# Kernel optimization log

Measured on AMD Instinct MI355X. Metric: run time of the kernel, lower is better.

## Reference

```python
import jax, jax.numpy as jnp
import numpy as np

B, S, T, D, H, K, F = 8, 512, 512, 1024, 16, 64, 4096
EPS = 1e-6
NEG = -1e9


def _ln(x, g, b):
    mu = jnp.mean(x, axis=-1, keepdims=True)
    var = jnp.mean(jnp.square(x - mu), axis=-1, keepdims=True)
    return (x - mu) * jax.lax.rsqrt(var + EPS) * g + b


def _mha(q_in, kv_in, wq, bq, wk, bk, wv, bv, wo, bo, mask=None):
    # q_in: [B,S,D], kv_in: [B,T,D]
    q = jnp.einsum('bsd,dhk->bshk', q_in, wq) + bq
    k = jnp.einsum('btd,dhk->bthk', kv_in, wk) + bk
    v = jnp.einsum('btd,dhk->bthk', kv_in, wv) + bv
    scores = jnp.einsum('bshk,bthk->bhst', q, k) / jnp.sqrt(jnp.float32(K))
    if mask is not None:
        scores = jnp.where(mask, scores, NEG)
    attn = jax.nn.softmax(scores, axis=-1)  # [B,H,S,T]
    ctx = jnp.einsum('bhst,bthk->bshk', attn, v)
    out = jnp.einsum('bshk,hkd->bsd', ctx, wo) + bo
    return out, attn


def setup_inputs() -> dict:
    key = jax.random.key(0)
    ks = jax.random.split(key, 24)
    r = lambda i, shape: 0.02 * jax.random.normal(ks[i], shape, dtype=jnp.float32)
    inp = {
        'x': jax.random.normal(ks[0], (B, S, D), dtype=jnp.float32),
        'enc_output': jax.random.normal(ks[1], (B, T, D), dtype=jnp.float32),
        'look_ahead_mask': jnp.tril(jnp.ones((S, S), dtype=bool))[None, None],
        # mha1 (self-attention)
        'wq1': r(2, (D, H, K)), 'bq1': jnp.zeros((H, K), jnp.float32),
        'wk1': r(3, (D, H, K)), 'bk1': jnp.zeros((H, K), jnp.float32),
        'wv1': r(4, (D, H, K)), 'bv1': jnp.zeros((H, K), jnp.float32),
        'wo1': r(5, (H, K, D)), 'bo1': jnp.zeros((D,), jnp.float32),
        # mha2 (cross-attention)
        'wq2': r(6, (D, H, K)), 'bq2': jnp.zeros((H, K), jnp.float32),
        'wk2': r(7, (D, H, K)), 'bk2': jnp.zeros((H, K), jnp.float32),
        'wv2': r(8, (D, H, K)), 'bv2': jnp.zeros((H, K), jnp.float32),
        'wo2': r(9, (H, K, D)), 'bo2': jnp.zeros((D,), jnp.float32),
        # layernorms
        'g1': jnp.ones((D,), jnp.float32), 'be1': jnp.zeros((D,), jnp.float32),
        'g2': jnp.ones((D,), jnp.float32), 'be2': jnp.zeros((D,), jnp.float32),
        'g3': jnp.ones((D,), jnp.float32), 'be3': jnp.zeros((D,), jnp.float32),
        # ffn
        'w_fc1': r(10, (D, F)), 'b_fc1': jnp.zeros((F,), jnp.float32),
        'w_fc2': r(11, (F, D)), 'b_fc2': jnp.zeros((D,), jnp.float32),
    }
    return inp


def reference(x, enc_output, look_ahead_mask,
              wq1, bq1, wk1, bk1, wv1, bv1, wo1, bo1,
              wq2, bq2, wk2, bk2, wv2, bv2, wo2, bo2,
              g1, be1, g2, be2, g3, be3,
              w_fc1, b_fc1, w_fc2, b_fc2):
    attn1, attn_w1 = _mha(x, x, wq1, bq1, wk1, bk1, wv1, bv1, wo1, bo1,
                          mask=look_ahead_mask)
    out1 = _ln(attn1 + x, g1, be1)
    attn2, attn_w2 = _mha(out1, enc_output, wq2, bq2, wk2, bk2, wv2, bv2, wo2, bo2)
    out2 = _ln(attn2 + out1, g2, be2)
    h = jax.nn.relu(jnp.einsum('bsd,df->bsf', out2, w_fc1) + b_fc1)
    out_ffn = jnp.einsum('bsf,fd->bsd', h, w_fc2) + b_fc2
    dec_layer_out = _ln(out_ffn + out2, g3, be3)
    return dec_layer_out, attn_w1, attn_w2
```

## Files before the change

kernel.cpp:

```cpp
#include <hip/hip_runtime.h>

typedef __attribute__((ext_vector_type(4))) float f32x4;
typedef __attribute__((ext_vector_type(8))) __bf16 bf16x8;

__device__ __forceinline__ unsigned short f2b(float f){
  union { float f; unsigned int u; } v; v.f = f;
  unsigned int r = v.u + 0x7FFFu + ((v.u >> 16) & 1u);
  return (unsigned short)(r >> 16);
}
__device__ __forceinline__ float b2f(unsigned short u){
  union { unsigned int u; float f; } v; v.u = ((unsigned int)u) << 16;
  return v.f;
}
__device__ __forceinline__ bool in_is_bf16(const void* g1){
  return ((const unsigned short*)g1)[0] == 0x3F80u;
}

#define GLD16(gp, lp) __builtin_amdgcn_global_load_lds( \
    (const __attribute__((address_space(1))) unsigned int*)(gp), \
    (__attribute__((address_space(3))) unsigned int*)(lp), 16, 0, 0)

__device__ __forceinline__ int xcd_swz(int L, int nwg){
  return (L & 7) * (nwg >> 3) + (L >> 3);
}

__global__ __launch_bounds__(256) void k_fill(float* p, long long n, float v){
  long long i = (long long)blockIdx.x*256 + threadIdx.x;
  long long stride = (long long)gridDim.x*256;
  for(; i < n; i += stride) p[i] = v;
}

struct SmallConv { const void* src[16]; int n[16]; int off[16]; };
struct TW4 { const void* s[4]; };

template<bool SMALL>
__global__ __launch_bounds__(256) void k_prepA(SmallConv sc, float* bias,
    const void* act_in, unsigned short* act_out,
    TW4 tw, unsigned short* wdst, const void* g1f)
{
  __shared__ float tile[32][33];
  bool isb = in_is_bf16(g1f);
  int bi = blockIdx.x, tid = threadIdx.x;
  int base = SMALL ? 16 : 0;
  if(SMALL && bi < 16){
    const void* s = sc.src[bi];
    float* d = bias + sc.off[bi];
    int n = sc.n[bi];
    for(int j=tid;j<n;j+=256)
      d[j] = isb ? b2f(((const unsigned short*)s)[j]) : ((const float*)s)[j];
  } else if(bi < base + 2048){
    for(int i=(bi-base)*256+tid; i<4194304; i+=2048*256){
      float v = isb ? b2f(((const unsigned short*)act_in)[i]) : ((const float*)act_in)[i];
      act_out[i] = f2b(v);
    }
  } else {
    int r = bi - (base + 2048);
    int wi = r >> 10, rem = r & 1023;
    int c0 = (rem & 31)*32, r0 = (rem >> 5)*32;
    const void* src = tw.s[wi];
    unsigned short* dst = wdst + (size_t)wi*1048576;
    int tx = tid & 31, ty = tid >> 5;
    for(int rr=ty; rr<32; rr+=8){
      size_t o = (size_t)(r0+rr)*1024 + c0 + tx;
      tile[rr][tx] = isb ? b2f(((const unsigned short*)src)[o]) : ((const float*)src)[o];
    }
    __syncthreads();
    for(int cc=ty; cc<32; cc+=8)
      dst[(size_t)(c0+cc)*1024 + r0 + tx] = f2b(tile[tx][cc]);
  }
}

__global__ __launch_bounds__(256) void k_prep3(
    const void* fc1, unsigned short* fc1t,
    const void* fc2, unsigned short* fc2t, const void* g1f)
{
  __shared__ float tile[32][33];
  bool isb = in_is_bf16(g1f);
  int bi = blockIdx.x, tid = threadIdx.x;
  const void* src; unsigned short* dst; int R, C, bx, by;
  if(bi < 4096){ src = fc1; dst = fc1t; R = 1024; C = 4096; bx = bi & 127; by = bi >> 7; }
  else { int r = bi - 4096; src = fc2; dst = fc2t; R = 4096; C = 1024; bx = r & 31; by = r >> 5; }
  int c0 = bx*32, r0 = by*32;
  int tx = tid & 31, ty = tid >> 5;
  for(int rr=ty; rr<32; rr+=8){
    size_t o = (size_t)(r0+rr)*C + c0 + tx;
    tile[rr][tx] = isb ? b2f(((const unsigned short*)src)[o]) : ((const float*)src)[o];
  }
  __syncthreads();
  for(int cc=ty; cc<32; cc+=8)
    dst[(size_t)(c0+cc)*R + r0 + tx] = f2b(tile[tx][cc]);
}

template<int EPI>
__global__ __launch_bounds__(512) void k_gemm256(
    const unsigned short* __restrict__ A, int lda,
    const unsigned short* __restrict__ Bt, int ldb,
    void* __restrict__ Cout, int ldc,
    const float* __restrict__ bias, const unsigned short* __restrict__ resid, int K)
{
  __shared__ __align__(16) unsigned short LA[2][256*64];
  __shared__ __align__(16) unsigned short LB[2][256*64];
  int tid = threadIdx.x;
  int lane = tid & 63;
  int lr = lane & 15, lg = lane >> 4;
  int w = tid >> 6, wr = w >> 2, wc = w & 3;
  int nwg = gridDim.x * gridDim.y;
  int v = xcd_swz(blockIdx.y * gridDim.x + blockIdx.x, nwg);
  int bx = v % gridDim.x, by = v / gridDim.x;
  int m0 = by * 256, n0 = bx * 256;
  int NT = K >> 6;

  f32x4 acc[8][4];
  #pragma unroll
  for(int m=0;m<8;m++)
    #pragma unroll
    for(int n=0;n<4;n++) acc[m][n] = (f32x4){0.f,0.f,0.f,0.f};

  #define STEP256(kt, sg) { \
    int sb_ = (kt) & 1; \
    _Pragma("unroll") \
    for(int jj=0;jj<2;jj++){ \
      int c_ = (((sg)&1)*2 + jj)*512 + tid; \
      int s_ = c_ ^ ((c_ >> 3) & 7); \
      if(((sg) & 2) == 0) \
        GLD16(A + (size_t)(m0 + (s_>>3))*lda + (kt)*64 + (s_&7)*8, \
              LA[sb_] + (size_t)c_*8); \
      else \
        GLD16(Bt + (size_t)(n0 + (s_>>3))*ldb + (kt)*64 + (s_&7)*8, \
              LB[sb_] + (size_t)c_*8); \
    } }

  #pragma unroll
  for(int sg=0;sg<4;sg++) STEP256(0, sg);
  if(NT > 1){
    #pragma unroll
    for(int sg=0;sg<4;sg++) STEP256(1, sg);
    asm volatile("s_waitcnt vmcnt(8)" ::: "memory");
  } else {
    asm volatile("s_waitcnt vmcnt(0)" ::: "memory");
  }
  __builtin_amdgcn_s_barrier();

  for(int kt = 0; kt < NT; ++kt){
    int cur = kt & 1;
    #pragma unroll
    for(int q=0;q<4;q++){
      bf16x8 afr[2][2], bfr[4][2];
      #pragma unroll
      for(int i=0;i<2;i++){
        int row = wr*128 + (2*q+i)*16 + lr;
        #pragma unroll
        for(int ks=0;ks<2;ks++){
          int ch = (row*8 + ks*4 + lg) ^ (row & 7);
          afr[i][ks] = *(const bf16x8*)(LA[cur] + (size_t)ch*8);
        }
      }
      #pragma unroll
      for(int n=0;n<4;n++){
        int row = wc*64 + n*16 + lr;
        #pragma unroll
        for(int ks=0;ks<2;ks++){
          int ch = (row*8 + ks*4 + lg) ^ (row & 7);
          bfr[n][ks] = *(const bf16x8*)(LB[cur] + (size_t)ch*8);
        }
      }
      int P = kt*4 + q;
      if(P >= 3){
        int k2 = (P+5) >> 2, sg = (P+5) & 3;
        if(k2 < NT) STEP256(k2, sg);
      }
      __builtin_amdgcn_s_barrier();
      __builtin_amdgcn_s_setprio(1);
      #pragma unroll
      for(int i=0;i<2;i++)
        #pragma unroll
        for(int n=0;n<4;n++)
          #pragma unroll
          for(int ks=0;ks<2;ks++)
            acc[2*q+i][n] = __builtin_amdgcn_mfma_f32_16x16x32_bf16(
                afr[i][ks], bfr[n][ks], acc[2*q+i][n], 0,0,0);
      __builtin_amdgcn_s_setprio(0);
      __builtin_amdgcn_s_barrier();
    }
    if(kt + 1 < NT){
      if(kt + 2 < NT) asm volatile("s_waitcnt vmcnt(2)" ::: "memory");
      else            asm volatile("s_waitcnt vmcnt(0)" ::: "memory");
      __builtin_amdgcn_s_barrier();
    }
  }
  #undef STEP256

  #pragma unroll
  for(int m=0;m<8;m++){
    #pragma unroll
    for(int n=0;n<4;n++){
      int col = n0 + wc*64 + n*16 + lr;
      float bb = bias[col];
      #pragma unroll
      for(int r=0;r<4;r++){
        int row = m0 + wr*128 + m*16 + lg*4 + r;
        size_t o = (size_t)row*ldc + col;
        float v2 = acc[m][n][r] + bb;
        if constexpr (EPI == 0){
          ((unsigned short*)Cout)[o] = f2b(v2);
        } else if constexpr (EPI == 1){
          ((unsigned short*)Cout)[o] = f2b(v2 > 0.f ? v2 : 0.f);
        } else if constexpr (EPI == 2){
          ((unsigned short*)Cout)[o] = f2b(v2 + b2f(resid[o]));
        } else {
          ((float*)Cout)[o] = v2 + b2f(resid[o]);
        }
      }
    }
  }
}

template<int EPI>
__global__ __launch_bounds__(256) void k_gemm64(
    const unsigned short* __restrict__ A, int lda,
    const unsigned short* __restrict__ Bt, int ldb,
    void* __restrict__ Cout, int ldc,
    const float* __restrict__ bias, const unsigned short* __restrict__ resid, int K)
{
  __shared__ unsigned short As[2][128*32];
  __shared__ unsigned short Bs[2][64*32];
  int tid = threadIdx.x, lane = tid & 63, w = tid >> 6;
  int lr = lane & 15, lg = lane >> 4;
  int nwg = gridDim.x * gridDim.y;
  int v = xcd_swz(blockIdx.y * gridDim.x + blockIdx.x, nwg);
  int bx = v % gridDim.x, by = v / gridDim.x;
  int m0 = by * 128, n0 = bx * 64;

  f32x4 acc[2][4];
  #pragma unroll
  for(int m=0;m<2;m++)
    #pragma unroll
    for(int n=0;n<4;n++) acc[m][n] = (f32x4){0.f,0.f,0.f,0.f};

  #pragma unroll
  for(int j=0;j<2;j++){
    int idx = j*256 + tid;
    GLD16(A + (size_t)(m0 + (idx>>2))*lda + (idx&3)*8,
          As[0] + (size_t)(j*256 + (tid & 192))*8);
  }
  GLD16(Bt + (size_t)(n0 + (tid>>2))*ldb + (tid&3)*8,
        Bs[0] + (size_t)(tid & 192)*8);
  __syncthreads();

  int cur = 0;
  for(int k0 = 0; k0 < K; k0 += 32){
    if(k0 + 32 < K){
      #pragma unroll
      for(int j=0;j<2;j++){
        int idx = j*256 + tid;
        GLD16(A + (size_t)(m0 + (idx>>2))*lda + k0 + 32 + (idx&3)*8,
              As[cur^1] + (size_t)(j*256 + (tid & 192))*8);
      }
      GLD16(Bt + (size_t)(n0 + (tid>>2))*ldb + k0 + 32 + (tid&3)*8,
            Bs[cur^1] + (size_t)(tid & 192)*8);
    }
    bf16x8 a[2], bf[4];
    #pragma unroll
    for(int m=0;m<2;m++) a[m] = *(const bf16x8*)&As[cur][(w*32 + m*16 + lr)*32 + lg*8];
    #pragma unroll
    for(int n=0;n<4;n++) bf[n] = *(const bf16x8*)&Bs[cur][(n*16 + lr)*32 + lg*8];
    #pragma unroll
    for(int m=0;m<2;m++)
      #pragma unroll
      for(int n=0;n<4;n++)
        acc[m][n] = __builtin_amdgcn_mfma_f32_16x16x32_bf16(a[m], bf[n], acc[m][n], 0,0,0);
    __syncthreads();
    cur ^= 1;
  }

  #pragma unroll
  for(int m=0;m<2;m++){
    #pragma unroll
    for(int n=0;n<4;n++){
      int col = n0 + n*16 + lr;
      float bb = bias[col];
      #pragma unroll
      for(int r=0;r<4;r++){
        int row = m0 + w*32 + m*16 + lg*4 + r;
        size_t o = (size_t)row*ldc + col;
        float v2 = acc[m][n][r] + bb;
        if constexpr (EPI == 0){
          ((unsigned short*)Cout)[o] = f2b(v2);
        } else if constexpr (EPI == 1){
          ((unsigned short*)Cout)[o] = f2b(v2 > 0.f ? v2 : 0.f);
        } else if constexpr (EPI == 2){
          ((unsigned short*)Cout)[o] = f2b(v2 + b2f(resid[o]));
        } else {
          ((float*)Cout)[o] = v2 + b2f(resid[o]);
        }
      }
    }
  }
}

template<int TSLOT>
__global__ __launch_bounds__(256) void k_gemmsplit(
    const unsigned short* __restrict__ A,
    const unsigned short* __restrict__ A2, int lda,
    const unsigned short* __restrict__ Bt, int ldb,
    unsigned short* __restrict__ C0, unsigned short* __restrict__ C1,
    unsigned short* __restrict__ C2,
    const float* __restrict__ bias, int K)
{
  __shared__ unsigned short As[2][128*32];
  __shared__ unsigned short Bs[2][128*32];
  int tid = threadIdx.x;
  int lane = tid & 63, w = tid >> 6;
  int lr = lane & 15, lg = lane >> 4;
  int nwg = gridDim.x * gridDim.y;
  int v = xcd_swz(blockIdx.y * gridDim.x + blockIdx.x, nwg);
  int bx = v % gridDim.x, by = v / gridDim.x;
  int m0 = by * 128, n0 = bx * 128;
  int wr = w >> 1, wc = w & 1;
  int slot = n0 >> 10;
  unsigned short* Cs = slot == 0 ? C0 : (slot == 1 ? C1 : C2);
  const unsigned short* Au = (slot == 0) ? A2 : A;
  int nl0 = n0 & 1023;

  f32x4 acc[4][4];
  #pragma unroll
  for(int m=0;m<4;m++)
    #pragma unroll
    for(int n=0;n<4;n++) acc[m][n] = (f32x4){0.f,0.f,0.f,0.f};

  #pragma unroll
  for(int j=0;j<2;j++){
    int idx = j*256 + tid;
    GLD16(Au + (size_t)(m0 + (idx>>2))*lda + (idx&3)*8,
          As[0] + (size_t)(j*256 + (tid & 192))*8);
    GLD16(Bt + (size_t)(n0 + (idx>>2))*ldb + (idx&3)*8,
          Bs[0] + (size_t)(j*256 + (tid & 192))*8);
  }
  __syncthreads();

  int cur = 0;
  for(int k0 = 0; k0 < K; k0 += 32){
    if(k0 + 32 < K){
      #pragma unroll
      for(int j=0;j<2;j++){
        int idx = j*256 + tid;
        GLD16(Au + (size_t)(m0 + (idx>>2))*lda + k0 + 32 + (idx&3)*8,
              As[cur^1] + (size_t)(j*256 + (tid & 192))*8);
        GLD16(Bt + (size_t)(n0 + (idx>>2))*ldb + k0 + 32 + (idx&3)*8,
              Bs[cur^1] + (size_t)(j*256 + (tid & 192))*8);
      }
    }
    bf16x8 a[4], b[4];
    #pragma unroll
    for(int m=0;m<4;m++) a[m] = *(const bf16x8*)&As[cur][(wr*64 + m*16 + lr)*32 + lg*8];
    #pragma unroll
    for(int n=0;n<4;n++) b[n] = *(const bf16x8*)&Bs[cur][(wc*64 + n*16 + lr)*32 + lg*8];
    #pragma unroll
    for(int m=0;m<4;m++)
      #pragma unroll
      for(int n=0;n<4;n++)
        acc[m][n] = __builtin_amdgcn_mfma_f32_16x16x32_bf16(a[m], b[n], acc[m][n], 0,0,0);
    __syncthreads();
    cur ^= 1;
  }

  if(slot != TSLOT){
    #pragma unroll
    for(int m=0;m<4;m++){
      #pragma unroll
      for(int n=0;n<4;n++){
        int coll = nl0 + wc*64 + n*16 + lr;
        float bb = bias[n0 + wc*64 + n*16 + lr];
        #pragma unroll
        for(int r=0;r<4;r++){
          int row = m0 + wr*64 + m*16 + lg*4 + r;
          Cs[(size_t)row*1024 + coll] = f2b(acc[m][n][r] + bb);
        }
      }
    }
  } else {
    #pragma unroll
    for(int m=0;m<4;m++){
      #pragma unroll
      for(int n=0;n<4;n++){
        int vcol = nl0 + wc*64 + n*16 + lr;
        float bb = bias[n0 + wc*64 + n*16 + lr];
        int rowb = m0 + wr*64 + m*16 + lg*4;
        int z = (rowb >> 9)*16 + (vcol >> 6);
        unsigned short tmp[4];
        #pragma unroll
        for(int r=0;r<4;r++) tmp[r] = f2b(acc[m][n][r] + bb);
        *(ushort4*)&Cs[((size_t)(z*64 + (vcol & 63)))*512 + (rowb & 511)] = *(ushort4*)tmp;
      }
    }
  }
}

template<bool CAUSAL>
__global__ __launch_bounds__(256) void k_attnf(
    const unsigned short* Q,
    const unsigned short* __restrict__ Km,
    const unsigned short* __restrict__ Vt,
    float* __restrict__ P,
    unsigned short* C)
{
  int tid = threadIdx.x, lane = tid & 63, w = tid >> 6;
  int lr = lane & 15, lg = lane >> 4;
  int L = (blockIdx.z * 16 + blockIdx.y) * 16 + blockIdx.x;
  int v = xcd_swz(L, 2048);
  int s0 = (v & 15) * 32;
  int h = (v >> 4) & 15;
  int b = v >> 8;
  int z = b*16 + h;
  const unsigned short* Qb = Q + ((size_t)(b*512 + s0))*1024 + h*64;
  const unsigned short* Kb = Km + ((size_t)(b*512))*1024 + h*64;
  float* Pb = P + ((size_t)(z*512 + s0))*512;

  __shared__ unsigned short P_lds[32*520];
  __shared__ float redm[32][4];
  __shared__ float reds[32][4];

  bf16x8 aq[2][2];
  #pragma unroll
  for(int m=0;m<2;m++)
    #pragma unroll
    for(int kk=0;kk<2;kk++)
      aq[m][kk] = *(const bf16x8*)(Qb + (size_t)(m*16 + lr)*1024 + kk*32 + lg*8);

  f32x4 sc[2][8];
  #pragma unroll
  for(int m=0;m<2;m++)
    #pragma unroll
    for(int cb=0;cb<8;cb++) sc[m][cb] = (f32x4){0.f,0.f,0.f,0.f};

  __builtin_amdgcn_s_setprio(1);
  #pragma unroll
  for(int cb=0; cb<8; cb++){
    int col = w*128 + cb*16 + lr;
    #pragma unroll
    for(int kk=0; kk<2; kk++){
      bf16x8 bq = *(const bf16x8*)(Kb + (size_t)col*1024 + kk*32 + lg*8);
      #pragma unroll
      for(int m=0;m<2;m++)
        sc[m][cb] = __builtin_amdgcn_mfma_f32_16x16x32_bf16(aq[m][kk], bq, sc[m][cb], 0,0,0);
    }
  }
  __builtin_amdgcn_s_setprio(0);

  #pragma unroll
  for(int m=0;m<2;m++)
    #pragma unroll
    for(int cb=0;cb<8;cb++)
      #pragma unroll
      for(int r=0;r<4;r++){
        int row_l = m*16 + lg*4 + r;
        int col = w*128 + cb*16 + lr;
        float sv = sc[m][cb][r] * 0.125f;
        if(CAUSAL && col > s0 + row_l) sv = -1e9f;
        sc[m][cb][r] = sv;
      }

  float gmax[2][4];
  #pragma unroll
  for(int m=0;m<2;m++)
    #pragma unroll
    for(int r=0;r<4;r++){
      float pm = -1e30f;
      #pragma unroll
      for(int cb=0;cb<8;cb++) pm = fmaxf(pm, sc[m][cb][r]);
      #pragma unroll
      for(int off=1; off<16; off<<=1) pm = fmaxf(pm, __shfl_xor(pm, off));
      if(lr == 0) redm[m*16 + lg*4 + r][w] = pm;
    }
  __syncthreads();
  #pragma unroll
  for(int m=0;m<2;m++)
    #pragma unroll
    for(int r=0;r<4;r++){
      int row_l = m*16 + lg*4 + r;
      gmax[m][r] = fmaxf(fmaxf(redm[row_l][0], redm[row_l][1]),
                         fmaxf(redm[row_l][2], redm[row_l][3]));
    }
  #pragma unroll
  for(int m=0;m<2;m++)
    #pragma unroll
    for(int r=0;r<4;r++){
      float ps = 0.f;
      #pragma unroll
      for(int cb=0;cb<8;cb++){
        float e = __expf(sc[m][cb][r] - gmax[m][r]);
        sc[m][cb][r] = e;
        ps += e;
      }
      #pragma unroll
      for(int off=1; off<16; off<<=1) ps += __shfl_xor(ps, off);
      if(lr == 0) reds[m*16 + lg*4 + r][w] = ps;
    }
  __syncthreads();
  #pragma unroll
  for(int m=0;m<2;m++)
    #pragma unroll
    for(int r=0;r<4;r++){
      int row_l = m*16 + lg*4 + r;
      float inv = 1.f / (reds[row_l][0] + reds[row_l][1] + reds[row_l][2] + reds[row_l][3]);
      #pragma unroll
      for(int cb=0;cb<8;cb++){
        int col = w*128 + cb*16 + lr;
        float p = sc[m][cb][r] * inv;
        Pb[(size_t)row_l*512 + col] = p;
        P_lds[row_l*520 + col] = f2b(p);
      }
    }
  __syncthreads();

  const unsigned short* Vb = Vt + ((size_t)z*64 + w*16 + lr)*512;
  f32x4 pacc[2];
  pacc[0] = (f32x4){0.f,0.f,0.f,0.f};
  pacc[1] = (f32x4){0.f,0.f,0.f,0.f};
  __builtin_amdgcn_s_setprio(1);
  for(int kk = 0; kk < 16; kk++){
    bf16x8 bfrag = *(const bf16x8*)(Vb + kk*32 + lg*8);
    #pragma unroll
    for(int m=0;m<2;m++){
      bf16x8 afrag = *(const bf16x8*)&P_lds[(m*16 + lr)*520 + kk*32 + lg*8];
      pacc[m] = __builtin_amdgcn_mfma_f32_16x16x32_bf16(afrag, bfrag, pacc[m], 0,0,0);
    }
  }
  __builtin_amdgcn_s_setprio(0);
  #pragma unroll
  for(int m=0;m<2;m++)
    #pragma unroll
    for(int r=0;r<4;r++)
      C[((size_t)(b*512 + s0 + m*16 + lg*4 + r))*1024 + h*64 + w*16 + lr] = f2b(pacc[m][r]);
}

template<int F32IN, int F32OUT>
__global__ __launch_bounds__(256) void k_ln(const void* __restrict__ in,
    const float* __restrict__ g, const float* __restrict__ be,
    void* __restrict__ out)
{
  int row = blockIdx.x, tid = threadIdx.x;
  float v[4];
  if constexpr (F32IN){
    f32x4 u = *(const f32x4*)((const float*)in + (size_t)row*1024 + tid*4);
    v[0]=u[0]; v[1]=u[1]; v[2]=u[2]; v[3]=u[3];
  } else {
    uint2 u = *(const uint2*)((const unsigned short*)in + (size_t)row*1024 + tid*4);
    v[0] = b2f(u.x & 0xFFFF); v[1] = b2f(u.x >> 16);
    v[2] = b2f(u.y & 0xFFFF); v[3] = b2f(u.y >> 16);
  }
  float s = v[0]+v[1]+v[2]+v[3];
  float s2 = v[0]*v[0]+v[1]*v[1]+v[2]*v[2]+v[3]*v[3];
  #pragma unroll
  for(int off=1; off<64; off<<=1){ s += __shfl_xor(s, off); s2 += __shfl_xor(s2, off); }
  __shared__ float red[2][4];
  int w = tid >> 6;
  if((tid & 63) == 0){ red[0][w] = s; red[1][w] = s2; }
  __syncthreads();
  s  = red[0][0]+red[0][1]+red[0][2]+red[0][3];
  s2 = red[1][0]+red[1][1]+red[1][2]+red[1][3];
  float mu = s * (1.f/1024.f);
  float var = s2 * (1.f/1024.f) - mu*mu;
  float rstd = rsqrtf(var + 1e-6f);
  int c = tid*4;
  float y0 = (v[0]-mu)*rstd*g[c+0] + be[c+0];
  float y1 = (v[1]-mu)*rstd*g[c+1] + be[c+1];
  float y2 = (v[2]-mu)*rstd*g[c+2] + be[c+2];
  float y3 = (v[3]-mu)*rstd*g[c+3] + be[c+3];
  if constexpr (F32OUT){
    f32x4 o = {y0, y1, y2, y3};
    *(f32x4*)((float*)out + (size_t)row*1024 + c) = o;
  } else {
    unsigned int o0 = (unsigned int)f2b(y0) | ((unsigned int)f2b(y1) << 16);
    unsigned int o1 = (unsigned int)f2b(y2) | ((unsigned int)f2b(y3) << 16);
    *(uint2*)((unsigned short*)out + (size_t)row*1024 + c) = make_uint2(o0, o1);
  }
}

extern "C" void kernel_launch(void* const* d_in, const int* in_sizes, int n_in,
                              void* d_out, int out_size, void* d_ws, size_t ws_size,
                              hipStream_t stream)
{
  float* out0 = (float*)d_out;

  static const int exp_sizes[29] = {
    4194304, 4194304, 262144,
    1048576, 1024, 1048576, 1024, 1048576, 1024, 1048576, 1024,
    1048576, 1024, 1048576, 1024, 1048576, 1024, 1048576, 1024,
    1024, 1024, 1024, 1024, 1024, 1024,
    4194304, 4096, 4194304, 1024 };
  bool ok = (n_in == 29);
  if(ok) for(int i=0;i<29;i++) if(in_sizes[i] != exp_sizes[i]) { ok = false; break; }
  if(!ok){
    k_fill<<<2048,256,0,stream>>>(out0, (long long)out_size, 100.0f);
    return;
  }
  size_t nslots = ws_size > 131072 ? (ws_size - 131072) / 8388608 : 0;
  if(nslots < 5){
    k_fill<<<2048,256,0,stream>>>(out0, (long long)out_size, 200.0f);
    return;
  }
  bool bigws = nslots >= 9;

  const void* g1f = d_in[19];
  char* ws = (char*)d_ws;
  float* bias = (float*)(ws);
  unsigned short* SL[9];
  for(int i=0;i<9;i++) SL[i] = (unsigned short*)(ws + 131072 + (size_t)i*8388608);

  float* P1 = out0 + 4194304;
  float* P2 = P1 + 33554432;
  unsigned short* Q2buf = (unsigned short*)out0;

  SmallConv scv;
  const int si[16] = {4,6,8,10,12,14,16,18,19,20,21,22,23,24,26,28};
  const int sn[16] = {1024,1024,1024,1024,1024,1024,1024,1024,
                      1024,1024,1024,1024,1024,1024,4096,1024};
  const int so[16] = {0,1024,2048,3072,4096,5120,6144,7168,
                      8192,9216,10240,11264,12288,13312,14336,18432};
  for(int i=0;i<16;i++){ scv.src[i]=d_in[si[i]]; scv.n[i]=sn[i]; scv.off[i]=so[i]; }

  {
    TW4 tw{}; tw.s[0]=d_in[3]; tw.s[1]=d_in[5]; tw.s[2]=d_in[7]; tw.s[3]=d_in[9];
    k_prepA<true><<<6160,256,0,stream>>>(scv, bias, d_in[0], SL[0], tw, SL[1], g1f);
  }
  k_gemmsplit<2><<<dim3(24,32),256,0,stream>>>(SL[0], SL[0],1024, SL[1],1024,
                                               SL[2], SL[3], SL[4], bias+0, 1024);
  k_attnf<true><<<dim3(16,16,8),256,0,stream>>>(SL[2], SL[3], SL[4], P1, SL[2]);
  k_gemm64<2><<<dim3(16,32),256,0,stream>>>(SL[2],1024, SL[1]+3145728,1024,
                                            SL[3],1024, bias+3072, SL[0], 1024);
  k_ln<0,0><<<4096,256,0,stream>>>(SL[3], bias+8192, bias+9216, SL[4]);

  {
    TW4 tw{}; tw.s[0]=d_in[11]; tw.s[1]=d_in[13]; tw.s[2]=d_in[15]; tw.s[3]=d_in[17];
    k_prepA<false><<<6144,256,0,stream>>>(scv, bias, d_in[1], SL[0], tw, SL[1], g1f);
  }
  k_gemmsplit<2><<<dim3(24,32),256,0,stream>>>(SL[0], SL[4],1024, SL[1],1024,
                                               Q2buf, SL[2], SL[3], bias+4096, 1024);
  k_attnf<false><<<dim3(16,16,8),256,0,stream>>>(Q2buf, SL[2], SL[3], P2, SL[0]);
  k_gemm64<2><<<dim3(16,32),256,0,stream>>>(SL[0],1024, SL[1]+3145728,1024,
                                            SL[2],1024, bias+7168, SL[4], 1024);
  k_ln<0,0><<<4096,256,0,stream>>>(SL[2], bias+10240, bias+11264, SL[3]);

  k_prep3<<<8192,256,0,stream>>>(d_in[25], SL[4], d_in[27], SL[0], g1f);
  if(bigws){
    unsigned short* H = SL[5];
    k_gemm256<1><<<dim3(16,16),512,0,stream>>>(SL[3],1024, SL[4],1024, H,4096,
                                               bias+14336, nullptr, 1024);
    k_gemm64<3><<<dim3(16,32),256,0,stream>>>(H,4096, SL[0],4096, out0,1024, bias+18432, SL[3], 4096);
    k_ln<1,1><<<4096,256,0,stream>>>(out0, bias+12288, bias+13312, out0);
  } else {
    unsigned short* H = SL[1];
    for(int c=0;c<2;c++){
      unsigned short* arow = SL[3] + (size_t)c*2097152;
      float* orow = out0 + (size_t)c*2097152;
      k_gemm256<1><<<dim3(16,8),512,0,stream>>>(arow,1024, SL[4],1024, H,4096,
                                                bias+14336, nullptr, 1024);
      k_gemm64<3><<<dim3(16,16),256,0,stream>>>(H,4096, SL[0],4096, orow,1024, bias+18432, arow, 4096);
      k_ln<1,1><<<2048,256,0,stream>>>(orow, bias+12288, bias+13312, orow);
    }
  }
}
```

Before: 473.5 us.

## Move QKV projection GEMMs onto the pipelined 256x256 GEMM body

Replaces the simple 128x128 double-buffered QKV split GEMM with a 256x256-tile, 512-thread version. It shares the software-pipelined swizzled-LDS main loop of k_gemm256, now factored into a macro. The goal is more reuse per tile and better latency hiding in the projection GEMMs. The grid shrinks to 192 workgroups, which may underfill the 256 CUs. The change also drops the s_setprio hints around the MFMA loops in the attention kernel.

After: 440.6 us. 7.0% less time.

```diff
diff --git a/kernel.cpp b/kernel.cpp
--- a/kernel.cpp
+++ b/kernel.cpp
@@ -91,6 +91,80 @@
     dst[(size_t)(c0+cc)*R + r0 + tx] = f2b(tile[tx][cc]);
 }
 
+#define STEP256(Ap, Bp, lda_, ldb_, m0_, n0_, kt, sg) { \
+  int sb_ = (kt) & 1; \
+  _Pragma("unroll") \
+  for(int jj=0;jj<2;jj++){ \
+    int c_ = (((sg)&1)*2 + jj)*512 + tid; \
+    int s_ = c_ ^ ((c_ >> 3) & 7); \
+    if(((sg) & 2) == 0) \
+      GLD16((Ap) + (size_t)((m0_) + (s_>>3))*(lda_) + (kt)*64 + (s_&7)*8, \
+            LA[sb_] + (size_t)c_*8); \
+    else \
+      GLD16((Bp) + (size_t)((n0_) + (s_>>3))*(ldb_) + (kt)*64 + (s_&7)*8, \
+            LB[sb_] + (size_t)c_*8); \
+  } }
+
+#define GEMM256_BODY(Ap, Bp) \
+   \
+  _Pragma("unroll") \
+  for(int sg=0;sg<4;sg++) STEP256(Ap, Bp, lda, ldb, m0, n0, 0, sg); \
+  if(NT > 1){ \
+    _Pragma("unroll") \
+    for(int sg=0;sg<4;sg++) STEP256(Ap, Bp, lda, ldb, m0, n0, 1, sg); \
+    asm volatile("s_waitcnt vmcnt(8)" ::: "memory"); \
+  } else { \
+    asm volatile("s_waitcnt vmcnt(0)" ::: "memory"); \
+  } \
+  __builtin_amdgcn_s_barrier(); \
+  for(int kt = 0; kt < NT; ++kt){ \
+    int cur = kt & 1; \
+    _Pragma("unroll") \
+    for(int q=0;q<4;q++){ \
+      bf16x8 afr[2][2], bfr[4][2]; \
+      _Pragma("unroll") \
+      for(int i=0;i<2;i++){ \
+        int row = wr*128 + (2*q+i)*16 + lr; \
+        _Pragma("unroll") \
+        for(int ks=0;ks<2;ks++){ \
+          int ch = (row*8 + ks*4 + lg) ^ (row & 7); \
+          afr[i][ks] = *(const bf16x8*)(LA[cur] + (size_t)ch*8); \
+        } \
+      } \
+      _Pragma("unroll") \
+      for(int n=0;n<4;n++){ \
+        int row = wc*64 + n*16 + lr; \
+        _Pragma("unroll") \
+        for(int ks=0;ks<2;ks++){ \
+          int ch = (row*8 + ks*4 + lg) ^ (row & 7); \
+          bfr[n][ks] = *(const bf16x8*)(LB[cur] + (size_t)ch*8); \
+        } \
+      } \
+      int P = kt*4 + q; \
+      if(P >= 3){ \
+        int k2 = (P+5) >> 2, sg = (P+5) & 3; \
+        if(k2 < NT) STEP256(Ap, Bp, lda, ldb, m0, n0, k2, sg); \
+      } \
+      __builtin_amdgcn_s_barrier(); \
+      __builtin_amdgcn_s_setprio(1); \
+      _Pragma("unroll") \
+      for(int i=0;i<2;i++) \
+        _Pragma("unroll") \
+        for(int n=0;n<4;n++) \
+          _Pragma("unroll") \
+          for(int ks=0;ks<2;ks++) \
+            acc[2*q+i][n] = __builtin_amdgcn_mfma_f32_16x16x32_bf16( \
+                afr[i][ks], bfr[n][ks], acc[2*q+i][n], 0,0,0); \
+      __builtin_amdgcn_s_setprio(0); \
+      __builtin_amdgcn_s_barrier(); \
+    } \
+    if(kt + 1 < NT){ \
+      if(kt + 2 < NT) asm volatile("s_waitcnt vmcnt(2)" ::: "memory"); \
+      else            asm volatile("s_waitcnt vmcnt(0)" ::: "memory"); \
+      __builtin_amdgcn_s_barrier(); \
+    } \
+  }
+
 template<int EPI>
 __global__ __launch_bounds__(512) void k_gemm256(
     const unsigned short* __restrict__ A, int lda,
@@ -116,79 +190,7 @@
     #pragma unroll
     for(int n=0;n<4;n++) acc[m][n] = (f32x4){0.f,0.f,0.f,0.f};
 
-  #define STEP256(kt, sg) { \
-    int sb_ = (kt) & 1; \
-    _Pragma("unroll") \
-    for(int jj=0;jj<2;jj++){ \
-      int c_ = (((sg)&1)*2 + jj)*512 + tid; \
-      int s_ = c_ ^ ((c_ >> 3) & 7); \
-      if(((sg) & 2) == 0) \
-        GLD16(A + (size_t)(m0 + (s_>>3))*lda + (kt)*64 + (s_&7)*8, \
-              LA[sb_] + (size_t)c_*8); \
-      else \
-        GLD16(Bt + (size_t)(n0 + (s_>>3))*ldb + (kt)*64 + (s_&7)*8, \
-              LB[sb_] + (size_t)c_*8); \
-    } }
-
-  #pragma unroll
-  for(int sg=0;sg<4;sg++) STEP256(0, sg);
-  if(NT > 1){
-    #pragma unroll
-    for(int sg=0;sg<4;sg++) STEP256(1, sg);
-    asm volatile("s_waitcnt vmcnt(8)" ::: "memory");
-  } else {
-    asm volatile("s_waitcnt vmcnt(0)" ::: "memory");
-  }
-  __builtin_amdgcn_s_barrier();
-
-  for(int kt = 0; kt < NT; ++kt){
-    int cur = kt & 1;
-    #pragma unroll
-    for(int q=0;q<4;q++){
-      bf16x8 afr[2][2], bfr[4][2];
-      #pragma unroll
-      for(int i=0;i<2;i++){
-        int row = wr*128 + (2*q+i)*16 + lr;
-        #pragma unroll
-        for(int ks=0;ks<2;ks++){
-          int ch = (row*8 + ks*4 + lg) ^ (row & 7);
-          afr[i][ks] = *(const bf16x8*)(LA[cur] + (size_t)ch*8);
-        }
-      }
-      #pragma unroll
-      for(int n=0;n<4;n++){
-        int row = wc*64 + n*16 + lr;
-        #pragma unroll
-        for(int ks=0;ks<2;ks++){
-          int ch = (row*8 + ks*4 + lg) ^ (row & 7);
-          bfr[n][ks] = *(const bf16x8*)(LB[cur] + (size_t)ch*8);
-        }
-      }
-      int P = kt*4 + q;
-      if(P >= 3){
-        int k2 = (P+5) >> 2, sg = (P+5) & 3;
-        if(k2 < NT) STEP256(k2, sg);
-      }
-      __builtin_amdgcn_s_barrier();
-      __builtin_amdgcn_s_setprio(1);
-      #pragma unroll
-      for(int i=0;i<2;i++)
-        #pragma unroll
-        for(int n=0;n<4;n++)
-          #pragma unroll
-          for(int ks=0;ks<2;ks++)
-            acc[2*q+i][n] = __builtin_amdgcn_mfma_f32_16x16x32_bf16(
-                afr[i][ks], bfr[n][ks], acc[2*q+i][n], 0,0,0);
-      __builtin_amdgcn_s_setprio(0);
-      __builtin_amdgcn_s_barrier();
-    }
-    if(kt + 1 < NT){
-      if(kt + 2 < NT) asm volatile("s_waitcnt vmcnt(2)" ::: "memory");
-      else            asm volatile("s_waitcnt vmcnt(0)" ::: "memory");
-      __builtin_amdgcn_s_barrier();
-    }
-  }
-  #undef STEP256
+  GEMM256_BODY(A, Bt)
 
   #pragma unroll
   for(int m=0;m<8;m++){
@@ -215,6 +217,71 @@
   }
 }
 
+template<int TSLOT>
+__global__ __launch_bounds__(512) void k_gemmsplit256(
+    const unsigned short* __restrict__ A,
+    const unsigned short* __restrict__ A2, int lda,
+    const unsigned short* __restrict__ Bt, int ldb,
+    unsigned short* __restrict__ C0, unsigned short* __restrict__ C1,
+    unsigned short* __restrict__ C2,
+    const float* __restrict__ bias, int K)
+{
+  __shared__ __align__(16) unsigned short LA[2][256*64];
+  __shared__ __align__(16) unsigned short LB[2][256*64];
+  int tid = threadIdx.x;
+  int lane = tid & 63;
+  int lr = lane & 15, lg = lane >> 4;
+  int w = tid >> 6, wr = w >> 2, wc = w & 3;
+  int nwg = gridDim.x * gridDim.y;
+  int v = xcd_swz(blockIdx.y * gridDim.x + blockIdx.x, nwg);
+  int bx = v % gridDim.x, by = v / gridDim.x;
+  int m0 = by * 256, n0 = bx * 256;
+  int NT = K >> 6;
+  int slot = bx >> 2;
+  unsigned short* Cs = slot == 0 ? C0 : (slot == 1 ? C1 : C2);
+  const unsigned short* Au = (slot == 0) ? A2 : A;
+  int nl0 = (bx & 3) * 256;
+
+  f32x4 acc[8][4];
+  #pragma unroll
+  for(int m=0;m<8;m++)
+    #pragma unroll
+    for(int n=0;n<4;n++) acc[m][n] = (f32x4){0.f,0.f,0.f,0.f};
+
+  GEMM256_BODY(Au, Bt)
+
+  if(slot != TSLOT){
+    #pragma unroll
+    for(int m=0;m<8;m++){
+      #pragma unroll
+      for(int n=0;n<4;n++){
+        int coll = nl0 + wc*64 + n*16 + lr;
+        float bb = bias[bx*256 + wc*64 + n*16 + lr];
+        #pragma unroll
+        for(int r=0;r<4;r++){
+          int row = m0 + wr*128 + m*16 + lg*4 + r;
+          Cs[(size_t)row*1024 + coll] = f2b(acc[m][n][r] + bb);
+        }
+      }
+    }
+  } else {
+    #pragma unroll
+    for(int m=0;m<8;m++){
+      #pragma unroll
+      for(int n=0;n<4;n++){
+        int vcol = nl0 + wc*64 + n*16 + lr;
+        float bb = bias[bx*256 + wc*64 + n*16 + lr];
+        int rowb = m0 + wr*128 + m*16 + lg*4;
+        int z = (rowb >> 9)*16 + (vcol >> 6);
+        unsigned short tmp[4];
+        #pragma unroll
+        for(int r=0;r<4;r++) tmp[r] = f2b(acc[m][n][r] + bb);
+        *(ushort4*)&Cs[((size_t)(z*64 + (vcol & 63)))*512 + (rowb & 511)] = *(ushort4*)tmp;
+      }
+    }
+  }
+}
+
 template<int EPI>
 __global__ __launch_bounds__(256) void k_gemm64(
     const unsigned short* __restrict__ A, int lda,
@@ -298,104 +365,6 @@
   }
 }
 
-template<int TSLOT>
-__global__ __launch_bounds__(256) void k_gemmsplit(
-    const unsigned short* __restrict__ A,
-    const unsigned short* __restrict__ A2, int lda,
-    const unsigned short* __restrict__ Bt, int ldb,
-    unsigned short* __restrict__ C0, unsigned short* __restrict__ C1,
-    unsigned short* __restrict__ C2,
-    const float* __restrict__ bias, int K)
-{
-  __shared__ unsigned short As[2][128*32];
-  __shared__ unsigned short Bs[2][128*32];
-  int tid = threadIdx.x;
-  int lane = tid & 63, w = tid >> 6;
-  int lr = lane & 15, lg = lane >> 4;
-  int nwg = gridDim.x * gridDim.y;
-  int v = xcd_swz(blockIdx.y * gridDim.x + blockIdx.x, nwg);
-  int bx = v % gridDim.x, by = v / gridDim.x;
-  int m0 = by * 128, n0 = bx * 128;
-  int wr = w >> 1, wc = w & 1;
-  int slot = n0 >> 10;
-  unsigned short* Cs = slot == 0 ? C0 : (slot == 1 ? C1 : C2);
-  const unsigned short* Au = (slot == 0) ? A2 : A;
-  int nl0 = n0 & 1023;
-
-  f32x4 acc[4][4];
-  #pragma unroll
-  for(int m=0;m<4;m++)
-    #pragma unroll
-    for(int n=0;n<4;n++) acc[m][n] = (f32x4){0.f,0.f,0.f,0.f};
-
-  #pragma unroll
-  for(int j=0;j<2;j++){
-    int idx = j*256 + tid;
-    GLD16(Au + (size_t)(m0 + (idx>>2))*lda + (idx&3)*8,
-          As[0] + (size_t)(j*256 + (tid & 192))*8);
-    GLD16(Bt + (size_t)(n0 + (idx>>2))*ldb + (idx&3)*8,
-          Bs[0] + (size_t)(j*256 + (tid & 192))*8);
-  }
-  __syncthreads();
-
-  int cur = 0;
-  for(int k0 = 0; k0 < K; k0 += 32){
-    if(k0 + 32 < K){
-      #pragma unroll
-      for(int j=0;j<2;j++){
-        int idx = j*256 + tid;
-        GLD16(Au + (size_t)(m0 + (idx>>2))*lda + k0 + 32 + (idx&3)*8,
-              As[cur^1] + (size_t)(j*256 + (tid & 192))*8);
-        GLD16(Bt + (size_t)(n0 + (idx>>2))*ldb + k0 + 32 + (idx&3)*8,
-              Bs[cur^1] + (size_t)(j*256 + (tid & 192))*8);
-      }
-    }
-    bf16x8 a[4], b[4];
-    #pragma unroll
-    for(int m=0;m<4;m++) a[m] = *(const bf16x8*)&As[cur][(wr*64 + m*16 + lr)*32 + lg*8];
-    #pragma unroll
-    for(int n=0;n<4;n++) b[n] = *(const bf16x8*)&Bs[cur][(wc*64 + n*16 + lr)*32 + lg*8];
-    #pragma unroll
-    for(int m=0;m<4;m++)
-      #pragma unroll
-      for(int n=0;n<4;n++)
-        acc[m][n] = __builtin_amdgcn_mfma_f32_16x16x32_bf16(a[m], b[n], acc[m][n], 0,0,0);
-    __syncthreads();
-    cur ^= 1;
-  }
-
-  if(slot != TSLOT){
-    #pragma unroll
-    for(int m=0;m<4;m++){
-      #pragma unroll
-      for(int n=0;n<4;n++){
-        int coll = nl0 + wc*64 + n*16 + lr;
-        float bb = bias[n0 + wc*64 + n*16 + lr];
-        #pragma unroll
-        for(int r=0;r<4;r++){
-          int row = m0 + wr*64 + m*16 + lg*4 + r;
-          Cs[(size_t)row*1024 + coll] = f2b(acc[m][n][r] + bb);
-        }
-      }
-    }
-  } else {
-    #pragma unroll
-    for(int m=0;m<4;m++){
-      #pragma unroll
-      for(int n=0;n<4;n++){
-        int vcol = nl0 + wc*64 + n*16 + lr;
-        float bb = bias[n0 + wc*64 + n*16 + lr];
-        int rowb = m0 + wr*64 + m*16 + lg*4;
-        int z = (rowb >> 9)*16 + (vcol >> 6);
-        unsigned short tmp[4];
-        #pragma unroll
-        for(int r=0;r<4;r++) tmp[r] = f2b(acc[m][n][r] + bb);
-        *(ushort4*)&Cs[((size_t)(z*64 + (vcol & 63)))*512 + (rowb & 511)] = *(ushort4*)tmp;
-      }
-    }
-  }
-}
-
 template<bool CAUSAL>
 __global__ __launch_bounds__(256) void k_attnf(
     const unsigned short* Q,
@@ -433,7 +402,6 @@
     #pragma unroll
     for(int cb=0;cb<8;cb++) sc[m][cb] = (f32x4){0.f,0.f,0.f,0.f};
 
-  __builtin_amdgcn_s_setprio(1);
   #pragma unroll
   for(int cb=0; cb<8; cb++){
     int col = w*128 + cb*16 + lr;
@@ -445,7 +413,6 @@
         sc[m][cb] = __builtin_amdgcn_mfma_f32_16x16x32_bf16(aq[m][kk], bq, sc[m][cb], 0,0,0);
     }
   }
-  __builtin_amdgcn_s_setprio(0);
 
   #pragma unroll
   for(int m=0;m<2;m++)
@@ -517,7 +484,6 @@
   f32x4 pacc[2];
   pacc[0] = (f32x4){0.f,0.f,0.f,0.f};
   pacc[1] = (f32x4){0.f,0.f,0.f,0.f};
-  __builtin_amdgcn_s_setprio(1);
   for(int kk = 0; kk < 16; kk++){
     bf16x8 bfrag = *(const bf16x8*)(Vb + kk*32 + lg*8);
     #pragma unroll
@@ -526,7 +492,6 @@
       pacc[m] = __builtin_amdgcn_mfma_f32_16x16x32_bf16(afrag, bfrag, pacc[m], 0,0,0);
     }
   }
-  __builtin_amdgcn_s_setprio(0);
   #pragma unroll
   for(int m=0;m<2;m++)
     #pragma unroll
@@ -624,8 +589,8 @@
     TW4 tw{}; tw.s[0]=d_in[3]; tw.s[1]=d_in[5]; tw.s[2]=d_in[7]; tw.s[3]=d_in[9];
     k_prepA<true><<<6160,256,0,stream>>>(scv, bias, d_in[0], SL[0], tw, SL[1], g1f);
   }
-  k_gemmsplit<2><<<dim3(24,32),256,0,stream>>>(SL[0], SL[0],1024, SL[1],1024,
-                                               SL[2], SL[3], SL[4], bias+0, 1024);
+  k_gemmsplit256<2><<<dim3(12,16),512,0,stream>>>(SL[0], SL[0],1024, SL[1],1024,
+                                                  SL[2], SL[3], SL[4], bias+0, 1024);
   k_attnf<true><<<dim3(16,16,8),256,0,stream>>>(SL[2], SL[3], SL[4], P1, SL[2]);
   k_gemm64<2><<<dim3(16,32),256,0,stream>>>(SL[2],1024, SL[1]+3145728,1024,
                                             SL[3],1024, bias+3072, SL[0], 1024);
@@ -635,8 +600,8 @@
     TW4 tw{}; tw.s[0]=d_in[11]; tw.s[1]=d_in[13]; tw.s[2]=d_in[15]; tw.s[3]=d_in[17];
     k_prepA<false><<<6144,256,0,stream>>>(scv, bias, d_in[1], SL[0], tw, SL[1], g1f);
   }
-  k_gemmsplit<2><<<dim3(24,32),256,0,stream>>>(SL[0], SL[4],1024, SL[1],1024,
-                                               Q2buf, SL[2], SL[3], bias+4096, 1024);
+  k_gemmsplit256<2><<<dim3(12,16),512,0,stream>>>(SL[0], SL[4],1024, SL[1],1024,
+                                                  Q2buf, SL[2], SL[3], bias+4096, 1024);
   k_attnf<false><<<dim3(16,16,8),256,0,stream>>>(Q2buf, SL[2], SL[3], P2, SL[0]);
   k_gemm64<2><<<dim3(16,32),256,0,stream>>>(SL[0],1024, SL[1]+3145728,1024,
                                             SL[2],1024, bias+7168, SL[4], 1024);
```
